# Performance work log

Measured on AMD Instinct MI355X. Metric: run time of the kernel, lower is better.

Reference implementation:

```python
import jax, jax.numpy as jnp
import numpy as np

BLOCK_SIZE = 64


def setup_inputs() -> dict:
    key = jax.random.key(0)
    kq, kk, kv = jax.random.split(key, 3)
    B, H, S, D = 1, 16, 4096, 64
    return {
        "query": jax.random.normal(kq, (B, H, S, D), dtype=jnp.float32),
        "key": jax.random.normal(kk, (B, H, S, D), dtype=jnp.float32),
        "value": jax.random.normal(kv, (B, H, S, D), dtype=jnp.float32),
    }


def reference(query, key, value):
    # scores: [B,H,S,S], scaled by 1/sqrt(D)
    D = query.shape[-1]
    scale = 1.0 / jnp.sqrt(jnp.asarray(D, dtype=jnp.float32))
    scores = jnp.einsum("bhqd,bhkd->bhqk", query, key) * scale
    S = scores.shape[-1]
    # block-diagonal mask: 1 inside diagonal blocks, 0 elsewhere.
    # NOTE: original multiplies scores by the mask (off-block scores become 0,
    # NOT -inf) and then softmaxes over the full row — replicate exactly.
    blk = jnp.arange(S) // BLOCK_SIZE
    block_mask = (blk[:, None] == blk[None, :]).astype(scores.dtype)  # [S,S]
    scores = scores * block_mask
    weights = jax.nn.softmax(scores, axis=-1)
    return jnp.einsum("bhqk,bhkd->bhqd", weights, value)
```

## Files before the change

### kernel.cpp

```cpp
#include <hip/hip_runtime.h>

#define H_ 16
#define S_ 4096
#define D_ 64
#define BS_ 64
#define NB_ 64
#define NUNITS (H_*NB_)
#define SCALE_ 0.125f
#define NSLICE 16
#define ROWS_PER_SLICE (S_/NSLICE)


__global__ __launch_bounds__(256) void vsum_part(const float* __restrict__ V,
                                                 float* __restrict__ part) {
    const int blk = blockIdx.x;
    const int h = blk >> 4, sl = blk & 15;
    const int t = threadIdx.x;
    const int d4 = t & 15, rg = t >> 4;
    const float4* vp = (const float4*)(V + ((size_t)h * S_ + (size_t)sl * ROWS_PER_SLICE) * D_);
    float4 acc = make_float4(0.f, 0.f, 0.f, 0.f);
    for (int s = rg; s < ROWS_PER_SLICE; s += 16) {
        float4 v = vp[s * 16 + d4];
        acc.x += v.x; acc.y += v.y; acc.z += v.z; acc.w += v.w;
    }
    __shared__ float4 red[16][16];
    red[rg][d4] = acc;
    __syncthreads();
    if (rg == 0) {
        float4 s0 = red[0][d4];
        #pragma unroll
        for (int r = 1; r < 16; ++r) {
            float4 v = red[r][d4];
            s0.x += v.x; s0.y += v.y; s0.z += v.z; s0.w += v.w;
        }
        ((float4*)(part + (size_t)blk * D_))[d4] = s0;
    }
}

__global__ __launch_bounds__(64) void vsum_final(const float* __restrict__ part,
                                                 float* __restrict__ vtot) {
    const int h = blockIdx.x;
    const int d = threadIdx.x;
    float s = 0.f;
    #pragma unroll
    for (int sl = 0; sl < NSLICE; ++sl) s += part[(h * NSLICE + sl) * D_ + d];
    vtot[h * D_ + d] = s;
}

__global__ __launch_bounds__(256) void battn(const float* __restrict__ Q,
                                             const float* __restrict__ K,
                                             const float* __restrict__ V,
                                             const float* __restrict__ vtot,
                                             float* __restrict__ O) {
    const int unit = blockIdx.x;
    const int h = unit >> 6, b = unit & 63;
    const int t = threadIdx.x;
    const int tx = t & 15, ty = t >> 4;

    __shared__ float Qs[64][65];
    __shared__ float Ks[64][65];
    __shared__ float Vs[64][65];

    const size_t base = ((size_t)h * S_ + (size_t)b * BS_) * D_;
    const float4* q4 = (const float4*)(Q + base);
    const float4* k4 = (const float4*)(K + base);
    const float4* v4 = (const float4*)(V + base);

    #pragma unroll
    for (int it = 0; it < 4; ++it) {
        int idx = t + it * 256;
        int r = idx >> 4, c = (idx & 15) << 2;
        float4 qv = q4[idx];
        float4 kv = k4[idx];
        float4 vv = v4[idx];
        Qs[r][c] = qv.x; Qs[r][c + 1] = qv.y; Qs[r][c + 2] = qv.z; Qs[r][c + 3] = qv.w;
        Ks[r][c] = kv.x; Ks[r][c + 1] = kv.y; Ks[r][c + 2] = kv.z; Ks[r][c + 3] = kv.w;
        Vs[r][c] = vv.x; Vs[r][c + 1] = vv.y; Vs[r][c + 2] = vv.z; Vs[r][c + 3] = vv.w;
    }
    __syncthreads();

    float s[4][4];
    #pragma unroll
    for (int i = 0; i < 4; ++i)
        #pragma unroll
        for (int j = 0; j < 4; ++j) s[i][j] = 0.f;

    #pragma unroll 4
    for (int d = 0; d < 64; ++d) {
        float qv[4], kv[4];
        #pragma unroll
        for (int i = 0; i < 4; ++i) qv[i] = Qs[ty + 16 * i][d];
        #pragma unroll
        for (int j = 0; j < 4; ++j) kv[j] = Ks[tx + 16 * j][d];
        #pragma unroll
        for (int i = 0; i < 4; ++i)
            #pragma unroll
            for (int j = 0; j < 4; ++j) s[i][j] = fmaf(qv[i], kv[j], s[i][j]);
    }

    #pragma unroll
    for (int i = 0; i < 4; ++i)
        #pragma unroll
        for (int j = 0; j < 4; ++j) s[i][j] *= SCALE_;

    float em[4], inv[4];
    #pragma unroll
    for (int i = 0; i < 4; ++i) {
        float mx = fmaxf(fmaxf(s[i][0], s[i][1]), fmaxf(s[i][2], s[i][3]));
        #pragma unroll
        for (int off = 1; off < 16; off <<= 1) mx = fmaxf(mx, __shfl_xor(mx, off, 16));
        mx = fmaxf(mx, 0.f);
        em[i] = __expf(-mx);
        float zs = 0.f;
        #pragma unroll
        for (int j = 0; j < 4; ++j) {
            s[i][j] = __expf(s[i][j] - mx) - em[i];
            zs += s[i][j];
        }
        #pragma unroll
        for (int off = 1; off < 16; off <<= 1) zs += __shfl_xor(zs, off, 16);
        inv[i] = 1.0f / (zs + (float)S_ * em[i]);
    }

    __syncthreads();
    #pragma unroll
    for (int i = 0; i < 4; ++i)
        #pragma unroll
        for (int j = 0; j < 4; ++j)
            Qs[ty + 16 * i][tx + 16 * j] = s[i][j] * inv[i];
    __syncthreads();

    float o[4][4];
    #pragma unroll
    for (int i = 0; i < 4; ++i)
        #pragma unroll
        for (int j = 0; j < 4; ++j) o[i][j] = 0.f;

    #pragma unroll 4
    for (int k = 0; k < 64; ++k) {
        float pv[4], vv[4];
        #pragma unroll
        for (int i = 0; i < 4; ++i) pv[i] = Qs[ty + 16 * i][k];
        #pragma unroll
        for (int j = 0; j < 4; ++j) vv[j] = Vs[k][tx + 16 * j];
        #pragma unroll
        for (int i = 0; i < 4; ++i)
            #pragma unroll
            for (int j = 0; j < 4; ++j) o[i][j] = fmaf(pv[i], vv[j], o[i][j]);
    }

    const float* vt = vtot + h * D_;
    float vtd[4];
    #pragma unroll
    for (int j = 0; j < 4; ++j) vtd[j] = vt[tx + 16 * j];

    float* op = O + base;
    #pragma unroll
    for (int i = 0; i < 4; ++i) {
        float c = em[i] * inv[i];
        #pragma unroll
        for (int j = 0; j < 4; ++j)
            op[(ty + 16 * i) * D_ + tx + 16 * j] = o[i][j] + c * vtd[j];
    }
}

extern "C" void kernel_launch(void* const* d_in, const int* in_sizes, int n_in,
                              void* d_out, int out_size, void* d_ws, size_t ws_size,
                              hipStream_t stream) {
    const float* Q = (const float*)d_in[0];
    const float* K = (const float*)d_in[1];
    const float* V = (const float*)d_in[2];
    float* out = (float*)d_out;
    float* part = (float*)d_ws;
    float* vtot = part + (size_t)H_ * NSLICE * D_;

    vsum_part<<<H_ * NSLICE, 256, 0, stream>>>(V, part);
    vsum_final<<<H_, 64, 0, stream>>>(part, vtot);
    battn<<<NUNITS, 256, 0, stream>>>(Q, K, V, vtot, out);
}
```

Baseline: 114.7 us.

## Use bf16 split-precision MFMA for block-diagonal attention matmuls

Replaces the scalar FP32 FMA tiles for QK^T and PV with MFMA 16x16x32 bf16 instructions. Each FP32 operand is split into a bf16 high and low part, and three MFMAs per product approximate FP32 accuracy. Q and K fragments are loaded straight from global memory into registers. V is staged transposed in shared memory as hi/lo bf16, and P is written hi/lo to shared memory. The change also drops an LDS pass and one barrier, and adds an occupancy hint to launch_bounds, at the cost of some precision and extra conversion work.

New measurement: 103.5 us. 9.8% less time.

```diff
diff --git a/kernel.cpp b/kernel.cpp
--- a/kernel.cpp
+++ b/kernel.cpp
@@ -3,13 +3,24 @@
 #define H_ 16
 #define S_ 4096
 #define D_ 64
-#define BS_ 64
 #define NB_ 64
 #define NUNITS (H_*NB_)
-#define SCALE_ 0.125f
 #define NSLICE 16
 #define ROWS_PER_SLICE (S_/NSLICE)
 
+typedef __bf16 bf16x8 __attribute__((ext_vector_type(8)));
+typedef float f32x4 __attribute__((ext_vector_type(4)));
+
+static __device__ __forceinline__ f32x4 mfma16(bf16x8 a, bf16x8 b, f32x4 c) {
+    return __builtin_amdgcn_mfma_f32_16x16x32_bf16(a, b, c, 0, 0, 0);
+}
+
+#define SPLIT1(x, hv, lv, idx) { float _x = (x); __bf16 _h = (__bf16)_x; (hv)[idx] = _h; (lv)[idx] = (__bf16)(_x - (float)_h); }
+
+static __device__ __forceinline__ void split8(float4 a, float4 b, bf16x8& hi, bf16x8& lo) {
+    SPLIT1(a.x, hi, lo, 0) SPLIT1(a.y, hi, lo, 1) SPLIT1(a.z, hi, lo, 2) SPLIT1(a.w, hi, lo, 3)
+    SPLIT1(b.x, hi, lo, 4) SPLIT1(b.y, hi, lo, 5) SPLIT1(b.z, hi, lo, 6) SPLIT1(b.w, hi, lo, 7)
+}
 
 __global__ __launch_bounds__(256) void vsum_part(const float* __restrict__ V,
                                                  float* __restrict__ part) {
@@ -47,120 +58,133 @@
     vtot[h * D_ + d] = s;
 }
 
-__global__ __launch_bounds__(256) void battn(const float* __restrict__ Q,
-                                             const float* __restrict__ K,
-                                             const float* __restrict__ V,
-                                             const float* __restrict__ vtot,
-                                             float* __restrict__ O) {
+__global__ __launch_bounds__(256, 3) void battn(const float* __restrict__ Q,
+                                                const float* __restrict__ K,
+                                                const float* __restrict__ V,
+                                                const float* __restrict__ vtot,
+                                                float* __restrict__ O) {
     const int unit = blockIdx.x;
     const int h = unit >> 6, b = unit & 63;
     const int t = threadIdx.x;
-    const int tx = t & 15, ty = t >> 4;
-
-    __shared__ float Qs[64][65];
-    __shared__ float Ks[64][65];
-    __shared__ float Vs[64][65];
-
-    const size_t base = ((size_t)h * S_ + (size_t)b * BS_) * D_;
-    const float4* q4 = (const float4*)(Q + base);
-    const float4* k4 = (const float4*)(K + base);
+    const int w = t >> 6;
+    const int lane = t & 63;
+    const int lr = lane & 15;
+    const int lg = lane >> 4;
+
+    __shared__ __bf16 VtH[64][72];
+    __shared__ __bf16 VtL[64][72];
+    __shared__ __bf16 PH[64][72];
+    __shared__ __bf16 PL[64][72];
+
+    const size_t base = ((size_t)h * S_ + (size_t)b * 64) * D_;
+
     const float4* v4 = (const float4*)(V + base);
-
     #pragma unroll
     for (int it = 0; it < 4; ++it) {
         int idx = t + it * 256;
-        int r = idx >> 4, c = (idx & 15) << 2;
-        float4 qv = q4[idx];
-        float4 kv = k4[idx];
+        int k  = idx >> 4;
+        int n0 = (idx & 15) << 2;
         float4 vv = v4[idx];
-        Qs[r][c] = qv.x; Qs[r][c + 1] = qv.y; Qs[r][c + 2] = qv.z; Qs[r][c + 3] = qv.w;
-        Ks[r][c] = kv.x; Ks[r][c + 1] = kv.y; Ks[r][c + 2] = kv.z; Ks[r][c + 3] = kv.w;
-        Vs[r][c] = vv.x; Vs[r][c + 1] = vv.y; Vs[r][c + 2] = vv.z; Vs[r][c + 3] = vv.w;
-    }
-    __syncthreads();
-
-    float s[4][4];
-    #pragma unroll
-    for (int i = 0; i < 4; ++i)
-        #pragma unroll
-        for (int j = 0; j < 4; ++j) s[i][j] = 0.f;
-
-    #pragma unroll 4
-    for (int d = 0; d < 64; ++d) {
-        float qv[4], kv[4];
-        #pragma unroll
-        for (int i = 0; i < 4; ++i) qv[i] = Qs[ty + 16 * i][d];
-        #pragma unroll
-        for (int j = 0; j < 4; ++j) kv[j] = Ks[tx + 16 * j][d];
-        #pragma unroll
-        for (int i = 0; i < 4; ++i)
-            #pragma unroll
-            for (int j = 0; j < 4; ++j) s[i][j] = fmaf(qv[i], kv[j], s[i][j]);
-    }
-
-    #pragma unroll
-    for (int i = 0; i < 4; ++i)
-        #pragma unroll
-        for (int j = 0; j < 4; ++j) s[i][j] *= SCALE_;
+        { float x = vv.x; __bf16 hh = (__bf16)x; VtH[n0+0][k] = hh; VtL[n0+0][k] = (__bf16)(x - (float)hh); }
+        { float x = vv.y; __bf16 hh = (__bf16)x; VtH[n0+1][k] = hh; VtL[n0+1][k] = (__bf16)(x - (float)hh); }
+        { float x = vv.z; __bf16 hh = (__bf16)x; VtH[n0+2][k] = hh; VtL[n0+2][k] = (__bf16)(x - (float)hh); }
+        { float x = vv.w; __bf16 hh = (__bf16)x; VtH[n0+3][k] = hh; VtL[n0+3][k] = (__bf16)(x - (float)hh); }
+    }
+
+    bf16x8 qh[2], ql[2];
+    {
+        const float* qrow = Q + base + (size_t)(w * 16 + lr) * D_;
+        #pragma unroll
+        for (int kk = 0; kk < 2; ++kk) {
+            const float4* p = (const float4*)(qrow + kk * 32 + lg * 8);
+            float4 a = p[0], c2 = p[1];
+            a.x *= 0.125f; a.y *= 0.125f; a.z *= 0.125f; a.w *= 0.125f;
+            c2.x *= 0.125f; c2.y *= 0.125f; c2.z *= 0.125f; c2.w *= 0.125f;
+            split8(a, c2, qh[kk], ql[kk]);
+        }
+    }
+
+    f32x4 acc[4];
+    #pragma unroll
+    for (int j = 0; j < 4; ++j) acc[j] = f32x4{0.f, 0.f, 0.f, 0.f};
+
+    #pragma unroll
+    for (int j = 0; j < 4; ++j) {
+        const float* krow = K + base + (size_t)(j * 16 + lr) * D_;
+        #pragma unroll
+        for (int kk = 0; kk < 2; ++kk) {
+            const float4* p = (const float4*)(krow + kk * 32 + lg * 8);
+            bf16x8 kh, kl;
+            split8(p[0], p[1], kh, kl);
+            acc[j] = mfma16(qh[kk], kh, acc[j]);
+            acc[j] = mfma16(ql[kk], kh, acc[j]);
+            acc[j] = mfma16(qh[kk], kl, acc[j]);
+        }
+    }
 
     float em[4], inv[4];
     #pragma unroll
-    for (int i = 0; i < 4; ++i) {
-        float mx = fmaxf(fmaxf(s[i][0], s[i][1]), fmaxf(s[i][2], s[i][3]));
+    for (int r = 0; r < 4; ++r) {
+        float mx = fmaxf(fmaxf(acc[0][r], acc[1][r]), fmaxf(acc[2][r], acc[3][r]));
         #pragma unroll
         for (int off = 1; off < 16; off <<= 1) mx = fmaxf(mx, __shfl_xor(mx, off, 16));
         mx = fmaxf(mx, 0.f);
-        em[i] = __expf(-mx);
-        float zs = 0.f;
+        float e = __expf(-mx);
+        float p0 = __expf(acc[0][r] - mx) - e;
+        float p1 = __expf(acc[1][r] - mx) - e;
+        float p2 = __expf(acc[2][r] - mx) - e;
+        float p3 = __expf(acc[3][r] - mx) - e;
+        float zs = p0 + p1 + p2 + p3;
+        #pragma unroll
+        for (int off = 1; off < 16; off <<= 1) zs += __shfl_xor(zs, off, 16);
+        float iv = 1.0f / (zs + 4096.0f * e);
+        em[r] = e; inv[r] = iv;
+        int row = w * 16 + lg * 4 + r;
+        { float pn = p0 * iv; __bf16 hh = (__bf16)pn; PH[row][lr +  0] = hh; PL[row][lr +  0] = (__bf16)(pn - (float)hh); }
+        { float pn = p1 * iv; __bf16 hh = (__bf16)pn; PH[row][lr + 16] = hh; PL[row][lr + 16] = (__bf16)(pn - (float)hh); }
+        { float pn = p2 * iv; __bf16 hh = (__bf16)pn; PH[row][lr + 32] = hh; PL[row][lr + 32] = (__bf16)(pn - (float)hh); }
+        { float pn = p3 * iv; __bf16 hh = (__bf16)pn; PH[row][lr + 48] = hh; PL[row][lr + 48] = (__bf16)(pn - (float)hh); }
+    }
+
+    __syncthreads();
+
+    bf16x8 pfh[2], pfl[2];
+    {
+        const int prow = w * 16 + lr;
+        #pragma unroll
+        for (int kk = 0; kk < 2; ++kk) {
+            pfh[kk] = *(const bf16x8*)&PH[prow][kk * 32 + lg * 8];
+            pfl[kk] = *(const bf16x8*)&PL[prow][kk * 32 + lg * 8];
+        }
+    }
+
+    f32x4 oacc[4];
+    #pragma unroll
+    for (int j = 0; j < 4; ++j) oacc[j] = f32x4{0.f, 0.f, 0.f, 0.f};
+
+    #pragma unroll
+    for (int j = 0; j < 4; ++j) {
+        #pragma unroll
+        for (int kk = 0; kk < 2; ++kk) {
+            bf16x8 vh = *(const bf16x8*)&VtH[lr + 16 * j][kk * 32 + lg * 8];
+            bf16x8 vl = *(const bf16x8*)&VtL[lr + 16 * j][kk * 32 + lg * 8];
+            oacc[j] = mfma16(pfh[kk], vh, oacc[j]);
+            oacc[j] = mfma16(pfl[kk], vh, oacc[j]);
+            oacc[j] = mfma16(pfh[kk], vl, oacc[j]);
+        }
+    }
+
+    const float* vt = vtot + h * D_;
+    float* op = O + base + (size_t)(w * 16) * D_;
+    #pragma unroll
+    for (int r = 0; r < 4; ++r) {
+        float c = em[r] * inv[r];
+        int row = lg * 4 + r;
         #pragma unroll
         for (int j = 0; j < 4; ++j) {
-            s[i][j] = __expf(s[i][j] - mx) - em[i];
-            zs += s[i][j];
-        }
-        #pragma unroll
-        for (int off = 1; off < 16; off <<= 1) zs += __shfl_xor(zs, off, 16);
-        inv[i] = 1.0f / (zs + (float)S_ * em[i]);
-    }
-
-    __syncthreads();
-    #pragma unroll
-    for (int i = 0; i < 4; ++i)
-        #pragma unroll
-        for (int j = 0; j < 4; ++j)
-            Qs[ty + 16 * i][tx + 16 * j] = s[i][j] * inv[i];
-    __syncthreads();
-
-    float o[4][4];
-    #pragma unroll
-    for (int i = 0; i < 4; ++i)
-        #pragma unroll
-        for (int j = 0; j < 4; ++j) o[i][j] = 0.f;
-
-    #pragma unroll 4
-    for (int k = 0; k < 64; ++k) {
-        float pv[4], vv[4];
-        #pragma unroll
-        for (int i = 0; i < 4; ++i) pv[i] = Qs[ty + 16 * i][k];
-        #pragma unroll
-        for (int j = 0; j < 4; ++j) vv[j] = Vs[k][tx + 16 * j];
-        #pragma unroll
-        for (int i = 0; i < 4; ++i)
-            #pragma unroll
-            for (int j = 0; j < 4; ++j) o[i][j] = fmaf(pv[i], vv[j], o[i][j]);
-    }
-
-    const float* vt = vtot + h * D_;
-    float vtd[4];
-    #pragma unroll
-    for (int j = 0; j < 4; ++j) vtd[j] = vt[tx + 16 * j];
-
-    float* op = O + base;
-    #pragma unroll
-    for (int i = 0; i < 4; ++i) {
-        float c = em[i] * inv[i];
-        #pragma unroll
-        for (int j = 0; j < 4; ++j)
-            op[(ty + 16 * i) * D_ + tx + 16 * j] = o[i][j] + c * vtd[j];
+            int col = lr + 16 * j;
+            op[row * D_ + col] = oacc[j][r] + c * vt[col];
+        }
     }
 }
 
```
